# Optimization experiments

Hardware: AMD Instinct MI355X
Metric: run time of the kernel (lower is better)

The kernel has to match this reference:

```python
import jax, jax.numpy as jnp
import numpy as np


def normalize_adj(adj):
    """Symmetrize (adj + adj.T*(adj.T>adj) - adj*(adj.T>adj)), add self loops, row-normalize D^-1 A."""
    at = jnp.swapaxes(adj, -1, -2)
    mask = (at > adj).astype(adj.dtype)
    a = adj + at * mask - adj * mask
    m = a.shape[-1]
    a = a + jnp.eye(m, dtype=a.dtype)
    rowsum = a.sum(axis=-1, keepdims=True)
    inv = jnp.where(rowsum > 0, 1.0 / rowsum, 0.0)
    return a * inv


def setup_inputs() -> dict:
    key = jax.random.key(0)
    ks = jax.random.split(key, 8)
    N, n, T, dim, M = 4, 3, 512, 2048, 256
    x = jax.random.normal(ks[0], (N, n, T, dim), dtype=jnp.float32)
    nodes = jax.random.normal(ks[1], (N, M, dim), dtype=jnp.float32)
    adj = (jax.random.uniform(ks[2], (N, M, M)) < 0.05).astype(jnp.float32)
    conv_w = jax.random.normal(ks[3], (2048, dim, 3), dtype=jnp.float32) * 0.02  # OIH
    conv_b = jnp.zeros((2048,), dtype=jnp.float32)
    W1 = jax.random.normal(ks[4], (dim, dim), dtype=jnp.float32) * 0.02
    b1 = jnp.zeros((dim,), dtype=jnp.float32)
    W2 = jax.random.normal(ks[5], (dim, dim), dtype=jnp.float32) * 0.02
    b2 = jnp.zeros((dim,), dtype=jnp.float32)
    return {"x": x, "nodes": nodes, "adj": adj, "conv_w": conv_w, "conv_b": conv_b,
            "W1": W1, "b1": b1, "W2": W2, "b2": b2}


def reference(x, nodes, adj, conv_w, conv_b, W1, b1, W2, b2):
    N, n, T, dim = x.shape
    # Conv1d front-end: (N*n, C=dim, T), kernel 3, pad 1, then ReLU
    feats = x.reshape(N * n, T, dim).transpose(0, 2, 1)  # [B, C, T]
    feats = jax.lax.conv_general_dilated(
        feats, conv_w, window_strides=(1,), padding=[(1, 1)],
        dimension_numbers=("NCH", "OIH", "NCH"))
    feats = jax.nn.relu(feats + conv_b[None, :, None])
    feats = feats.transpose(0, 2, 1).reshape(N, n, T, dim)
    # GCN_Module over per-sample node graphs (batched over N)
    a = normalize_adj(adj)                                   # [N, M, M]
    h = jax.nn.relu(jnp.einsum("bij,bjf->bif", a, nodes @ W1) + b1)
    out = jnp.einsum("bij,bjf->bif", a, h @ W2) + b2         # [N, M, dim]
    return feats, out
```

## Files before the change

### kernel.cpp

```cpp
#include <hip/hip_runtime.h>
#include <stdint.h>

typedef __bf16 bf16x8 __attribute__((ext_vector_type(8)));
typedef float floatx4 __attribute__((ext_vector_type(4)));

__device__ __forceinline__ void gload_lds16(const void* g, void* l) {
    __builtin_amdgcn_global_load_lds((const __attribute__((address_space(1))) void*)g,
                                     (__attribute__((address_space(3))) void*)l, 16, 0, 0);
}

__device__ __forceinline__ uint16_t f2bf(float f) {
    uint32_t u = __float_as_uint(f);
    u += 0x7fff + ((u >> 16) & 1);
    return (uint16_t)(u >> 16);
}
__device__ __forceinline__ uint32_t f2bf2(float lo, float hi) {
    return (uint32_t)f2bf(lo) | ((uint32_t)f2bf(hi) << 16);
}

#define PREP_A  1024
#define PREP_W  3072
#define PREP_T  5120
#define PREP_N  29792

__global__ __launch_bounds__(256)
void k_prep(const float* __restrict__ x, uint32_t* __restrict__ xpad,
            const float* __restrict__ w, uint16_t* __restrict__ wT,
            const float* __restrict__ W1, const float* __restrict__ W2,
            uint16_t* __restrict__ W1T, uint16_t* __restrict__ W2T,
            const float* __restrict__ adj, float* __restrict__ aval,
            uint16_t* __restrict__ aidx, int* __restrict__ annz)
{
    __shared__ union {
        float wbuf[6144];
        float tile[64][65];
        struct { float part[4]; int wcnt[4]; int woff[4]; float sinv; } na;
    } sm;
    const int bid = blockIdx.x;
    const int tid = threadIdx.x;

    if (bid < PREP_A) {
        int i = bid & 255, b = bid >> 8, j = tid;
        const float* A = adj + ((size_t)b << 16);
        float aij = A[(i << 8) + j];
        float aji = A[(j << 8) + i];
        float v = fmaxf(aij, aji);
        if (j == i) v += 1.0f;

        float s = v;
        #pragma unroll
        for (int off = 32; off > 0; off >>= 1) s += __shfl_down(s, off);

        bool pred = v != 0.0f;
        unsigned long long m = __ballot(pred);
        int wid = j >> 6;
        if ((j & 63) == 0) { sm.na.part[wid] = s; sm.na.wcnt[wid] = (int)__popcll(m); }
        __syncthreads();
        int row = (b << 8) + i;
        if (j == 0) {
            float tt = sm.na.part[0] + sm.na.part[1] + sm.na.part[2] + sm.na.part[3];
            sm.na.sinv = tt > 0.0f ? 1.0f / tt : 0.0f;
            int o = 0;
            #pragma unroll
            for (int ww = 0; ww < 4; ++ww) { sm.na.woff[ww] = o; o += sm.na.wcnt[ww]; }
            annz[row] = o;
        }
        __syncthreads();
        if (pred) {
            int pos = sm.na.woff[wid] + (int)__popcll(m & ((1ull << (j & 63)) - 1ull));
            aval[row * 256 + pos] = v * sm.na.sinv;
            aidx[row * 256 + pos] = (uint16_t)j;
        }
    } else if (bid < PREP_W) {
        int o = bid - PREP_A;
        const float* src = w + (size_t)o * 6144;
        uint16_t*    dst = wT + (size_t)o * 6144;
        #pragma unroll
        for (int it = 0; it < 24; ++it)
            sm.wbuf[it * 256 + tid] = src[it * 256 + tid];
        __syncthreads();
        #pragma unroll
        for (int h = 0; h < 3; ++h)
            #pragma unroll
            for (int c = 0; c < 8; ++c) {
                int i = c * 256 + tid;
                dst[h * 2048 + i] = f2bf(sm.wbuf[i * 3 + h]);
            }
    } else if (bid < PREP_T) {
        int t  = bid - PREP_W;
        int z  = t >> 10;
        int by = (t >> 5) & 31;
        int bx = t & 31;
        const float* src = z ? W2 : W1;
        uint16_t*    dst = z ? W2T : W1T;
        int tx = tid & 63, ty = tid >> 6;
        for (int rr = ty; rr < 64; rr += 4)
            sm.tile[rr][tx] = src[(size_t)(by * 64 + rr) * 2048 + bx * 64 + tx];
        __syncthreads();
        for (int rr = ty; rr < 64; rr += 4)
            dst[(size_t)(bx * 64 + rr) * 2048 + by * 64 + tx] = f2bf(sm.tile[tx][rr]);
    } else {
        int idx2 = (bid - PREP_T) * 256 + tid;
        int i2   = idx2 & 1023;
        int tmp  = idx2 >> 10;
        int b    = tmp / 514;
        int tt   = tmp - b * 514;
        float lo = 0.0f, hi = 0.0f;
        if (tt >= 1 && tt <= 512) {
            const float* s = x + ((size_t)(b * 512 + tt - 1) << 11) + i2 * 2;
            lo = s[0]; hi = s[1];
        }
        xpad[idx2] = f2bf2(lo, hi);
    }
}

template<bool CONV, bool RELU>
__global__ __launch_bounds__(256)
void k_gemm(const uint16_t* __restrict__ A, const uint16_t* __restrict__ BT,
            float* __restrict__ C, const float* __restrict__ bias,
            int N, int K)
{
    __shared__ __align__(16) uint16_t As[128 * 32];
    __shared__ __align__(16) uint16_t Bs[128 * 32];
    const int tid  = threadIdx.x;
    const int rt   = blockIdx.y * 128;
    const int ct   = blockIdx.x * 128;
    const int lane = tid & 63;
    const int wave = tid >> 6;
    const int wm   = (wave >> 1) * 64;
    const int wn   = (wave & 1) * 64;
    const int lm   = lane & 15;
    const int kq   = (lane >> 4) * 8;
    const int srow  = tid >> 2;
    const int skcol = (tid & 3) * 8;

    size_t abase[2], bbase[2];
    #pragma unroll
    for (int ii = 0; ii < 2; ++ii) {
        int row = ii * 64 + srow;
        if (CONV) {
            int r = rt + row;
            int b = r >> 9;
            int t = r & 511;
            abase[ii] = ((size_t)(b * 514 + t) << 11) + skcol;
        } else {
            abase[ii] = (size_t)(rt + row) * K + skcol;
        }
        bbase[ii] = (size_t)(ct + row) * K + skcol;
    }

    floatx4 acc[4][4] = {};

    for (int k0 = 0; k0 < K; k0 += 32) {
        #pragma unroll
        for (int ii = 0; ii < 2; ++ii) {
            gload_lds16(A  + abase[ii] + k0, &As[ii * 2048 + tid * 8]);
            gload_lds16(BT + bbase[ii] + k0, &Bs[ii * 2048 + tid * 8]);
        }
        __syncthreads();

        bf16x8 af[4], bfr[4];
        #pragma unroll
        for (int mt = 0; mt < 4; ++mt)
            af[mt] = *(const bf16x8*)&As[(wm + mt * 16 + lm) * 32 + kq];
        #pragma unroll
        for (int nt = 0; nt < 4; ++nt)
            bfr[nt] = *(const bf16x8*)&Bs[(wn + nt * 16 + lm) * 32 + kq];
        #pragma unroll
        for (int mt = 0; mt < 4; ++mt)
            #pragma unroll
            for (int nt = 0; nt < 4; ++nt)
                acc[mt][nt] = __builtin_amdgcn_mfma_f32_16x16x32_bf16(af[mt], bfr[nt], acc[mt][nt], 0, 0, 0);
        __syncthreads();
    }

    const int lq = lane >> 4;
    #pragma unroll
    for (int mt = 0; mt < 4; ++mt) {
        #pragma unroll
        for (int nt = 0; nt < 4; ++nt) {
            int col = ct + wn + nt * 16 + lm;
            float bv = bias[col];
            #pragma unroll
            for (int r = 0; r < 4; ++r) {
                int row = rt + wm + mt * 16 + lq * 4 + r;
                float v = acc[mt][nt][r] + bv;
                if (RELU) v = fmaxf(v, 0.0f);
                C[(size_t)row * N + col] = v;
            }
        }
    }
}

template<bool RELU>
__global__ __launch_bounds__(256)
void k_gemm64(const uint16_t* __restrict__ A, const uint16_t* __restrict__ BT,
              float* __restrict__ C, const float* __restrict__ bias,
              int N, int K)
{
    __shared__ __align__(16) uint16_t As[64 * 32];
    __shared__ __align__(16) uint16_t Bs[64 * 32];
    const int tid  = threadIdx.x;
    const int rt   = blockIdx.y * 64;
    const int ct   = blockIdx.x * 64;
    const int lane = tid & 63;
    const int wave = tid >> 6;
    const int wm   = (wave >> 1) * 32;
    const int wn   = (wave & 1) * 32;
    const int lm   = lane & 15;
    const int kq   = (lane >> 4) * 8;
    const int srow  = tid >> 2;
    const int skcol = (tid & 3) * 8;

    const size_t abase = (size_t)(rt + srow) * K + skcol;
    const size_t bbase = (size_t)(ct + srow) * K + skcol;

    floatx4 acc[2][2] = {};

    for (int k0 = 0; k0 < K; k0 += 32) {
        gload_lds16(A  + abase + k0, &As[tid * 8]);
        gload_lds16(BT + bbase + k0, &Bs[tid * 8]);
        __syncthreads();

        bf16x8 af[2], bfr[2];
        #pragma unroll
        for (int mt = 0; mt < 2; ++mt)
            af[mt] = *(const bf16x8*)&As[(wm + mt * 16 + lm) * 32 + kq];
        #pragma unroll
        for (int nt = 0; nt < 2; ++nt)
            bfr[nt] = *(const bf16x8*)&Bs[(wn + nt * 16 + lm) * 32 + kq];
        #pragma unroll
        for (int mt = 0; mt < 2; ++mt)
            #pragma unroll
            for (int nt = 0; nt < 2; ++nt)
                acc[mt][nt] = __builtin_amdgcn_mfma_f32_16x16x32_bf16(af[mt], bfr[nt], acc[mt][nt], 0, 0, 0);
        __syncthreads();
    }

    const int lq = lane >> 4;
    #pragma unroll
    for (int mt = 0; mt < 2; ++mt) {
        #pragma unroll
        for (int nt = 0; nt < 2; ++nt) {
            int col = ct + wn + nt * 16 + lm;
            float bv = bias[col];
            #pragma unroll
            for (int r = 0; r < 4; ++r) {
                int row = rt + wm + mt * 16 + lq * 4 + r;
                float v = acc[mt][nt][r] + bv;
                if (RELU) v = fmaxf(v, 0.0f);
                C[(size_t)row * N + col] = v;
            }
        }
    }
}

__global__ void k_amul(const float* __restrict__ aval, const uint16_t* __restrict__ aidx,
                       const int* __restrict__ annz, const float* __restrict__ H,
                       uint16_t* __restrict__ outp)
{
    int f = blockIdx.x * 256 + threadIdx.x;
    int i = blockIdx.y;
    int b = blockIdx.z;
    int row = (b << 8) + i;
    __shared__ float vv[256];
    __shared__ int   jj[256];
    int n0 = annz[row];
    vv[threadIdx.x] = aval[row * 256 + threadIdx.x];
    jj[threadIdx.x] = aidx[row * 256 + threadIdx.x];
    __syncthreads();
    const float* Hb = H + ((size_t)b << 8) * 2048;
    float s = 0.0f;
    #pragma unroll 4
    for (int c = 0; c < n0; ++c)
        s += vv[c] * Hb[(size_t)jj[c] * 2048 + f];
    outp[(size_t)row * 2048 + f] = f2bf(s);
}


extern "C" void kernel_launch(void* const* d_in, const int* in_sizes, int n_in,
                              void* d_out, int out_size, void* d_ws, size_t ws_size,
                              hipStream_t stream)
{
    const float* x      = (const float*)d_in[0];
    const float* nodes  = (const float*)d_in[1];
    const float* adj    = (const float*)d_in[2];
    const float* conv_w = (const float*)d_in[3];
    const float* conv_b = (const float*)d_in[4];
    const float* W1     = (const float*)d_in[5];
    const float* b1     = (const float*)d_in[6];
    const float* W2     = (const float*)d_in[7];
    const float* b2     = (const float*)d_in[8];
    float* out = (float*)d_out;

    char* ws = (char*)d_ws;
    uint16_t* xpad   = (uint16_t*)(ws);
    uint16_t* wmT    = (uint16_t*)(ws + 25288704);
    uint16_t* W1T    = (uint16_t*)(ws + 50454528);
    uint16_t* W2T    = (uint16_t*)(ws + 58843136);
    float*    aval   = (float*)   (ws + 67231744);
    uint16_t* aidx   = (uint16_t*)(ws + 68280320);
    int*      annz   = (int*)     (ws + 68804608);
    uint16_t* gbf    = (uint16_t*)(ws + 68808704);
    float*    h      = (float*)   (ws + 73003008);
    uint16_t* ahb    = (uint16_t*)(ws + 81391616);

    k_prep<<<PREP_N, 256, 0, stream>>>(x, (uint32_t*)xpad, conv_w, wmT,
                                       W1, W2, W1T, W2T,
                                       adj, aval, aidx, annz);

    k_gemm<true, true><<<dim3(16, 48), 256, 0, stream>>>(xpad, wmT, out, conv_b, 2048, 6144);

    k_amul<<<dim3(8, 256, 4), 256, 0, stream>>>(aval, aidx, annz, nodes, gbf);
    k_gemm64<true><<<dim3(32, 16), 256, 0, stream>>>(gbf, W1T, h, b1, 2048, 2048);
    k_amul<<<dim3(8, 256, 4), 256, 0, stream>>>(aval, aidx, annz, h, ahb);
    k_gemm64<false><<<dim3(32, 16), 256, 0, stream>>>(ahb, W2T, out + 12582912, b2, 2048, 2048);
}
```

Before: 470.1 us.

## Fuse adjacency normalization into sparse aggregation and merge conv GEMM with first GCN GEMM

The adjacency-normalize step is folded into each sparse A·H row block, so the compressed aval/aidx/annz buffers are no longer written out and read back. The first aggregation (A·nodes) moves into the prep kernel. The conv GEMM and the W1 GEMM now share one launch, with block ranges dispatched by index, cutting two launches and letting the small GEMM's blocks fill the tail of the large one. The aggregation is also vectorized to 8 features per thread with float4 loads. In exchange, the adjacency is renormalized in both aggregation passes, and the prep kernel's first 1024 blocks now do heavier gather work.

```diff
diff --git a/kernel.cpp b/kernel.cpp
--- a/kernel.cpp
+++ b/kernel.cpp
@@ -18,61 +18,97 @@
     return (uint32_t)f2bf(lo) | ((uint32_t)f2bf(hi) << 16);
 }
 
-#define PREP_A  1024
-#define PREP_W  3072
-#define PREP_T  5120
-#define PREP_N  29792
+struct AmulSM {
+    float vv[256];
+    int   jj[256];
+    float part[4];
+    int   wcnt[4];
+    int   woff[4];
+    float sinv;
+    int   n0;
+};
+
+__device__ __forceinline__ void amul_body(const float* __restrict__ adj,
+                                          const float* __restrict__ H,
+                                          uint16_t* __restrict__ outp,
+                                          int b, int i, int tid, AmulSM* sm)
+{
+    const float* A = adj + ((size_t)b << 16);
+    float aij = A[(i << 8) + tid];
+    float aji = A[(tid << 8) + i];
+    float v = fmaxf(aij, aji);
+    if (tid == i) v += 1.0f;
+
+    float s = v;
+    #pragma unroll
+    for (int off = 32; off > 0; off >>= 1) s += __shfl_down(s, off);
+
+    bool pred = v != 0.0f;
+    unsigned long long m = __ballot(pred);
+    int wid = tid >> 6;
+    if ((tid & 63) == 0) { sm->part[wid] = s; sm->wcnt[wid] = (int)__popcll(m); }
+    __syncthreads();
+    if (tid == 0) {
+        float t = sm->part[0] + sm->part[1] + sm->part[2] + sm->part[3];
+        sm->sinv = t > 0.0f ? 1.0f / t : 0.0f;
+        int o = 0;
+        #pragma unroll
+        for (int w = 0; w < 4; ++w) { sm->woff[w] = o; o += sm->wcnt[w]; }
+        sm->n0 = o;
+    }
+    __syncthreads();
+    if (pred) {
+        int pos = sm->woff[wid] + (int)__popcll(m & ((1ull << (tid & 63)) - 1ull));
+        sm->vv[pos] = v * sm->sinv;
+        sm->jj[pos] = tid;
+    }
+    __syncthreads();
+
+    const int n0 = sm->n0;
+    const int f0 = tid * 8;
+    const float* Hb = H + (((size_t)b) << 8) * 2048;
+    float acc[8] = {};
+    for (int c = 0; c < n0; ++c) {
+        float av = sm->vv[c];
+        const float* hp = Hb + (size_t)sm->jj[c] * 2048 + f0;
+        float4 p = *(const float4*)hp;
+        float4 q = *(const float4*)(hp + 4);
+        acc[0] += av * p.x; acc[1] += av * p.y; acc[2] += av * p.z; acc[3] += av * p.w;
+        acc[4] += av * q.x; acc[5] += av * q.y; acc[6] += av * q.z; acc[7] += av * q.w;
+    }
+    uint4 o;
+    o.x = f2bf2(acc[0], acc[1]);
+    o.y = f2bf2(acc[2], acc[3]);
+    o.z = f2bf2(acc[4], acc[5]);
+    o.w = f2bf2(acc[6], acc[7]);
+    *(uint4*)(outp + (((size_t)b << 8) + i) * 2048 + f0) = o;
+}
+
+#define PR_AM 1024
+#define PR_W  3072
+#define PR_T  5120
+#define PR_N  29792
 
 __global__ __launch_bounds__(256)
 void k_prep(const float* __restrict__ x, uint32_t* __restrict__ xpad,
             const float* __restrict__ w, uint16_t* __restrict__ wT,
             const float* __restrict__ W1, const float* __restrict__ W2,
             uint16_t* __restrict__ W1T, uint16_t* __restrict__ W2T,
-            const float* __restrict__ adj, float* __restrict__ aval,
-            uint16_t* __restrict__ aidx, int* __restrict__ annz)
+            const float* __restrict__ adj, const float* __restrict__ nodes,
+            uint16_t* __restrict__ gbf)
 {
     __shared__ union {
-        float wbuf[6144];
-        float tile[64][65];
-        struct { float part[4]; int wcnt[4]; int woff[4]; float sinv; } na;
+        float  wbuf[6144];
+        float  tile[64][65];
+        AmulSM am;
     } sm;
     const int bid = blockIdx.x;
     const int tid = threadIdx.x;
 
-    if (bid < PREP_A) {
-        int i = bid & 255, b = bid >> 8, j = tid;
-        const float* A = adj + ((size_t)b << 16);
-        float aij = A[(i << 8) + j];
-        float aji = A[(j << 8) + i];
-        float v = fmaxf(aij, aji);
-        if (j == i) v += 1.0f;
-
-        float s = v;
-        #pragma unroll
-        for (int off = 32; off > 0; off >>= 1) s += __shfl_down(s, off);
-
-        bool pred = v != 0.0f;
-        unsigned long long m = __ballot(pred);
-        int wid = j >> 6;
-        if ((j & 63) == 0) { sm.na.part[wid] = s; sm.na.wcnt[wid] = (int)__popcll(m); }
-        __syncthreads();
-        int row = (b << 8) + i;
-        if (j == 0) {
-            float tt = sm.na.part[0] + sm.na.part[1] + sm.na.part[2] + sm.na.part[3];
-            sm.na.sinv = tt > 0.0f ? 1.0f / tt : 0.0f;
-            int o = 0;
-            #pragma unroll
-            for (int ww = 0; ww < 4; ++ww) { sm.na.woff[ww] = o; o += sm.na.wcnt[ww]; }
-            annz[row] = o;
-        }
-        __syncthreads();
-        if (pred) {
-            int pos = sm.na.woff[wid] + (int)__popcll(m & ((1ull << (j & 63)) - 1ull));
-            aval[row * 256 + pos] = v * sm.na.sinv;
-            aidx[row * 256 + pos] = (uint16_t)j;
-        }
-    } else if (bid < PREP_W) {
-        int o = bid - PREP_A;
+    if (bid < PR_AM) {
+        amul_body(adj, nodes, gbf, bid >> 8, bid & 255, tid, &sm.am);
+    } else if (bid < PR_W) {
+        int o = bid - PR_AM;
         const float* src = w + (size_t)o * 6144;
         uint16_t*    dst = wT + (size_t)o * 6144;
         #pragma unroll
@@ -86,8 +122,8 @@
                 int i = c * 256 + tid;
                 dst[h * 2048 + i] = f2bf(sm.wbuf[i * 3 + h]);
             }
-    } else if (bid < PREP_T) {
-        int t  = bid - PREP_W;
+    } else if (bid < PR_T) {
+        int t  = bid - PR_W;
         int z  = t >> 10;
         int by = (t >> 5) & 31;
         int bx = t & 31;
@@ -100,7 +136,7 @@
         for (int rr = ty; rr < 64; rr += 4)
             dst[(size_t)(bx * 64 + rr) * 2048 + by * 64 + tx] = f2bf(sm.tile[tx][rr]);
     } else {
-        int idx2 = (bid - PREP_T) * 256 + tid;
+        int idx2 = (bid - PR_T) * 256 + tid;
         int i2   = idx2 & 1023;
         int tmp  = idx2 >> 10;
         int b    = tmp / 514;
@@ -114,89 +150,137 @@
     }
 }
 
-template<bool CONV, bool RELU>
 __global__ __launch_bounds__(256)
-void k_gemm(const uint16_t* __restrict__ A, const uint16_t* __restrict__ BT,
-            float* __restrict__ C, const float* __restrict__ bias,
-            int N, int K)
-{
-    __shared__ __align__(16) uint16_t As[128 * 32];
-    __shared__ __align__(16) uint16_t Bs[128 * 32];
+void k_big(const uint16_t* __restrict__ xpad, const uint16_t* __restrict__ wmT,
+           float* __restrict__ feats, const float* __restrict__ conv_b,
+           const uint16_t* __restrict__ gbf, const uint16_t* __restrict__ W1T,
+           float* __restrict__ h, const float* __restrict__ b1)
+{
+    __shared__ __align__(16) uint16_t lds[8192];
+    const int bid  = blockIdx.x;
     const int tid  = threadIdx.x;
-    const int rt   = blockIdx.y * 128;
-    const int ct   = blockIdx.x * 128;
     const int lane = tid & 63;
     const int wave = tid >> 6;
-    const int wm   = (wave >> 1) * 64;
-    const int wn   = (wave & 1) * 64;
     const int lm   = lane & 15;
     const int kq   = (lane >> 4) * 8;
+    const int lq   = lane >> 4;
     const int srow  = tid >> 2;
     const int skcol = (tid & 3) * 8;
 
-    size_t abase[2], bbase[2];
-    #pragma unroll
-    for (int ii = 0; ii < 2; ++ii) {
-        int row = ii * 64 + srow;
-        if (CONV) {
-            int r = rt + row;
-            int b = r >> 9;
-            int t = r & 511;
-            abase[ii] = ((size_t)(b * 514 + t) << 11) + skcol;
-        } else {
-            abase[ii] = (size_t)(rt + row) * K + skcol;
+    if (bid < 768) {
+        uint16_t* As = lds;
+        uint16_t* Bs = lds + 4096;
+        const int rt = (bid >> 4) * 128;
+        const int ct = (bid & 15) * 128;
+        const int wm = (wave >> 1) * 64;
+        const int wn = (wave & 1) * 64;
+
+        floatx4 acc[4][4] = {};
+
+        for (int k0 = 0; k0 < 6144; k0 += 32) {
+            #pragma unroll
+            for (int ii = 0; ii < 2; ++ii) {
+                int row = ii * 64 + srow;
+                int r  = rt + row;
+                int b  = r >> 9;
+                int t  = r & 511;
+                int kk = k0 + skcol;
+                int hh = kk >> 11;
+                int ic = kk & 2047;
+                gload_lds16(xpad + ((size_t)(b * 514 + t + hh) << 11) + ic,
+                            &As[ii * 2048 + tid * 8]);
+                gload_lds16(wmT + (size_t)(ct + row) * 6144 + k0 + skcol,
+                            &Bs[ii * 2048 + tid * 8]);
+            }
+            __syncthreads();
+
+            bf16x8 af[4], bfr[4];
+            #pragma unroll
+            for (int mt = 0; mt < 4; ++mt)
+                af[mt] = *(const bf16x8*)&As[(wm + mt * 16 + lm) * 32 + kq];
+            #pragma unroll
+            for (int nt = 0; nt < 4; ++nt)
+                bfr[nt] = *(const bf16x8*)&Bs[(wn + nt * 16 + lm) * 32 + kq];
+            #pragma unroll
+            for (int mt = 0; mt < 4; ++mt)
+                #pragma unroll
+                for (int nt = 0; nt < 4; ++nt)
+                    acc[mt][nt] = __builtin_amdgcn_mfma_f32_16x16x32_bf16(af[mt], bfr[nt], acc[mt][nt], 0, 0, 0);
+            __syncthreads();
         }
-        bbase[ii] = (size_t)(ct + row) * K + skcol;
-    }
-
-    floatx4 acc[4][4] = {};
-
-    for (int k0 = 0; k0 < K; k0 += 32) {
-        #pragma unroll
-        for (int ii = 0; ii < 2; ++ii) {
-            gload_lds16(A  + abase[ii] + k0, &As[ii * 2048 + tid * 8]);
-            gload_lds16(BT + bbase[ii] + k0, &Bs[ii * 2048 + tid * 8]);
+
+        #pragma unroll
+        for (int mt = 0; mt < 4; ++mt)
+            #pragma unroll
+            for (int nt = 0; nt < 4; ++nt) {
+                int col = ct + wn + nt * 16 + lm;
+                float bv = conv_b[col];
+                #pragma unroll
+                for (int r = 0; r < 4; ++r) {
+                    int row = rt + wm + mt * 16 + lq * 4 + r;
+                    feats[(size_t)row * 2048 + col] = fmaxf(acc[mt][nt][r] + bv, 0.0f);
+                }
+            }
+    } else {
+        uint16_t* As = lds;
+        uint16_t* Bs = lds + 2048;
+        const int t  = bid - 768;
+        const int rt = (t >> 5) * 64;
+        const int ct = (t & 31) * 64;
+        const int wm = (wave >> 1) * 32;
+        const int wn = (wave & 1) * 32;
+
+        const size_t abase = (size_t)(rt + srow) * 2048 + skcol;
+        const size_t bbase = (size_t)(ct + srow) * 2048 + skcol;
+
+        floatx4 acc[2][2] = {};
+
+        for (int k0 = 0; k0 < 2048; k0 += 32) {
+            gload_lds16(gbf + abase + k0, &As[tid * 8]);
+            gload_lds16(W1T + bbase + k0, &Bs[tid * 8]);
+            __syncthreads();
+
+            bf16x8 af[2], bfr[2];
+            #pragma unroll
+            for (int mt = 0; mt < 2; ++mt)
+                af[mt] = *(const bf16x8*)&As[(wm + mt * 16 + lm) * 32 + kq];
+            #pragma unroll
+            for (int nt = 0; nt < 2; ++nt)
+                bfr[nt] = *(const bf16x8*)&Bs[(wn + nt * 16 + lm) * 32 + kq];
+            #pragma unroll
+            for (int mt = 0; mt < 2; ++mt)
+                #pragma unroll
+                for (int nt = 0; nt < 2; ++nt)
+                    acc[mt][nt] = __builtin_amdgcn_mfma_f32_16x16x32_bf16(af[mt], bfr[nt], acc[mt][nt], 0, 0, 0);
+            __syncthreads();
         }
-        __syncthreads();
-
-        bf16x8 af[4], bfr[4];
-        #pragma unroll
-        for (int mt = 0; mt < 4; ++mt)
-            af[mt] = *(const bf16x8*)&As[(wm + mt * 16 + lm) * 32 + kq];
-        #pragma unroll
-        for (int nt = 0; nt < 4; ++nt)
-            bfr[nt] = *(const bf16x8*)&Bs[(wn + nt * 16 + lm) * 32 + kq];
-        #pragma unroll
-        for (int mt = 0; mt < 4; ++mt)
-            #pragma unroll
-            for (int nt = 0; nt < 4; ++nt)
-                acc[mt][nt] = __builtin_amdgcn_mfma_f32_16x16x32_bf16(af[mt], bfr[nt], acc[mt][nt], 0, 0, 0);
-        __syncthreads();
-    }
-
-    const int lq = lane >> 4;
-    #pragma unroll
-    for (int mt = 0; mt < 4; ++mt) {
-        #pragma unroll
-        for (int nt = 0; nt < 4; ++nt) {
-            int col = ct + wn + nt * 16 + lm;
-            float bv = bias[col];
-            #pragma unroll
-            for (int r = 0; r < 4; ++r) {
-                int row = rt + wm + mt * 16 + lq * 4 + r;
-                float v = acc[mt][nt][r] + bv;
-                if (RELU) v = fmaxf(v, 0.0f);
-                C[(size_t)row * N + col] = v;
-            }
-        }
-    }
-}
-
-template<bool RELU>
+
+        #pragma unroll
+        for (int mt = 0; mt < 2; ++mt)
+            #pragma unroll
+            for (int nt = 0; nt < 2; ++nt) {
+                int col = ct + wn + nt * 16 + lm;
+                float bv = b1[col];
+                #pragma unroll
+                for (int r = 0; r < 4; ++r) {
+                    int row = rt + wm + mt * 16 + lq * 4 + r;
+                    h[(size_t)row * 2048 + col] = fmaxf(acc[mt][nt][r] + bv, 0.0f);
+                }
+            }
+    }
+}
+
+__global__ __launch_bounds__(256)
+void k_amul(const float* __restrict__ adj, const float* __restrict__ H,
+            uint16_t* __restrict__ outp)
+{
+    __shared__ AmulSM sm;
+    amul_body(adj, H, outp, blockIdx.x >> 8, blockIdx.x & 255, threadIdx.x, &sm);
+}
+
 __global__ __launch_bounds__(256)
 void k_gemm64(const uint16_t* __restrict__ A, const uint16_t* __restrict__ BT,
-              float* __restrict__ C, const float* __restrict__ bias,
-              int N, int K)
+              float* __restrict__ C, const float* __restrict__ bias)
 {
     __shared__ __align__(16) uint16_t As[64 * 32];
     __shared__ __align__(16) uint16_t Bs[64 * 32];
@@ -212,12 +296,12 @@
     const int srow  = tid >> 2;
     const int skcol = (tid & 3) * 8;
 
-    const size_t abase = (size_t)(rt + srow) * K + skcol;
-    const size_t bbase = (size_t)(ct + srow) * K + skcol;
+    const size_t abase = (size_t)(rt + srow) * 2048 + skcol;
+    const size_t bbase = (size_t)(ct + srow) * 2048 + skcol;
 
     floatx4 acc[2][2] = {};
 
-    for (int k0 = 0; k0 < K; k0 += 32) {
+    for (int k0 = 0; k0 < 2048; k0 += 32) {
         gload_lds16(A  + abase + k0, &As[tid * 8]);
         gload_lds16(BT + bbase + k0, &Bs[tid * 8]);
         __syncthreads();
@@ -239,7 +323,7 @@
 
     const int lq = lane >> 4;
     #pragma unroll
-    for (int mt = 0; mt < 2; ++mt) {
+    for (int mt = 0; mt < 2; ++mt)
         #pragma unroll
         for (int nt = 0; nt < 2; ++nt) {
             int col = ct + wn + nt * 16 + lm;
@@ -247,34 +331,9 @@
             #pragma unroll
             for (int r = 0; r < 4; ++r) {
                 int row = rt + wm + mt * 16 + lq * 4 + r;
-                float v = acc[mt][nt][r] + bv;
-                if (RELU) v = fmaxf(v, 0.0f);
-                C[(size_t)row * N + col] = v;
+                C[(size_t)row * 2048 + col] = acc[mt][nt][r] + bv;
             }
         }
-    }
-}
-
-__global__ void k_amul(const float* __restrict__ aval, const uint16_t* __restrict__ aidx,
-                       const int* __restrict__ annz, const float* __restrict__ H,
-                       uint16_t* __restrict__ outp)
-{
-    int f = blockIdx.x * 256 + threadIdx.x;
-    int i = blockIdx.y;
-    int b = blockIdx.z;
-    int row = (b << 8) + i;
-    __shared__ float vv[256];
-    __shared__ int   jj[256];
-    int n0 = annz[row];
-    vv[threadIdx.x] = aval[row * 256 + threadIdx.x];
-    jj[threadIdx.x] = aidx[row * 256 + threadIdx.x];
-    __syncthreads();
-    const float* Hb = H + ((size_t)b << 8) * 2048;
-    float s = 0.0f;
-    #pragma unroll 4
-    for (int c = 0; c < n0; ++c)
-        s += vv[c] * Hb[(size_t)jj[c] * 2048 + f];
-    outp[(size_t)row * 2048 + f] = f2bf(s);
 }
 
 
@@ -298,21 +357,13 @@
     uint16_t* wmT    = (uint16_t*)(ws + 25288704);
     uint16_t* W1T    = (uint16_t*)(ws + 50454528);
     uint16_t* W2T    = (uint16_t*)(ws + 58843136);
-    float*    aval   = (float*)   (ws + 67231744);
-    uint16_t* aidx   = (uint16_t*)(ws + 68280320);
-    int*      annz   = (int*)     (ws + 68804608);
-    uint16_t* gbf    = (uint16_t*)(ws + 68808704);
-    float*    h      = (float*)   (ws + 73003008);
-    uint16_t* ahb    = (uint16_t*)(ws + 81391616);
-
-    k_prep<<<PREP_N, 256, 0, stream>>>(x, (uint32_t*)xpad, conv_w, wmT,
-                                       W1, W2, W1T, W2T,
-                                       adj, aval, aidx, annz);
-
-    k_gemm<true, true><<<dim3(16, 48), 256, 0, stream>>>(xpad, wmT, out, conv_b, 2048, 6144);
-
-    k_amul<<<dim3(8, 256, 4), 256, 0, stream>>>(aval, aidx, annz, nodes, gbf);
-    k_gemm64<true><<<dim3(32, 16), 256, 0, stream>>>(gbf, W1T, h, b1, 2048, 2048);
-    k_amul<<<dim3(8, 256, 4), 256, 0, stream>>>(aval, aidx, annz, h, ahb);
-    k_gemm64<false><<<dim3(32, 16), 256, 0, stream>>>(ahb, W2T, out + 12582912, b2, 2048, 2048);
-}
+    uint16_t* gbf    = (uint16_t*)(ws + 67231744);
+    float*    h      = (float*)   (ws + 71426048);
+    uint16_t* ahb    = (uint16_t*)(ws + 79814656);
+
+    k_prep<<<PR_N, 256, 0, stream>>>(x, (uint32_t*)xpad, conv_w, wmT,
+                                     W1, W2, W1T, W2T, adj, nodes, gbf);
+    k_big<<<1280, 256, 0, stream>>>(xpad, wmT, out, conv_b, gbf, W1T, h, b1);
+    k_amul<<<1024, 256, 0, stream>>>(adj, h, ahb);
+    k_gemm64<<<dim3(32, 16), 256, 0, stream>>>(ahb, W2T, out + 12582912, b2);
+}
```

Result: faster. 427.5 us (-9.1%).
